# Kernel tuning notes

Measured on AMD Instinct MI355X. Metric: run time of the kernel, lower is better.

## Reference

```python
import jax, jax.numpy as jnp
import numpy as np

B, S, D, H = 4, 2048, 1024, 16
HD = D // H  # head size = 64

def setup_inputs() -> dict:
    key = jax.random.key(0)
    ks = jax.random.split(key, 9)
    s = 1.0 / np.sqrt(D)
    inp = {"x": jax.random.normal(ks[0], (B, S, D), dtype=jnp.float32)}
    for i, n in enumerate(["q", "k", "v", "o"]):
        inp[f"W{n}"] = jax.random.uniform(ks[1 + 2 * i], (D, D), minval=-s, maxval=s, dtype=jnp.float32)
        inp[f"b{n}"] = jax.random.uniform(ks[2 + 2 * i], (D,), minval=-s, maxval=s, dtype=jnp.float32)
    return inp

def reference(x, Wq, bq, Wk, bk, Wv, bv, Wo, bo):
    b, s, d = x.shape
    # project and split heads: [b, h, s, hd]
    def heads(y):
        return y.reshape(b, s, H, HD).transpose(0, 2, 1, 3)
    q = heads(x @ Wq.T + bq)
    k = heads(x @ Wk.T + bk)
    v = heads(x @ Wv.T + bv)
    scores = jnp.einsum('bhqd,bhkd->bhqk', q, k) / jnp.sqrt(jnp.float32(HD))
    attn = jax.nn.softmax(scores, axis=-1)
    ctx = jnp.einsum('bhqk,bhkd->bhqd', attn, v)
    ctx = ctx.transpose(0, 2, 1, 3).reshape(b, s, d)
    return ctx @ Wo.T + bo
```

## Files before the change

### kernel.cpp

```cpp
#include <hip/hip_runtime.h>
#include <hip/hip_bf16.h>

typedef __bf16 bf16;
typedef __bf16 bf16x8 __attribute__((ext_vector_type(8)));
typedef __bf16 bf16x4 __attribute__((ext_vector_type(4)));
typedef float f32x4 __attribute__((ext_vector_type(4)));
typedef float f32x16 __attribute__((ext_vector_type(16)));
typedef unsigned int u32;
typedef u32 u32x4 __attribute__((ext_vector_type(4)));

#define B_ 4
#define S_ 2048
#define D_ 1024
#define H_ 16
#define HD_ 64
#define LOG2E 1.4426950408889634f

static __device__ __forceinline__ f32x4 mfma16(bf16x8 a, bf16x8 b, f32x4 c) {
  return __builtin_amdgcn_mfma_f32_16x16x32_bf16(a, b, c, 0, 0, 0);
}
static __device__ __forceinline__ f32x16 mfma32(bf16x8 a, bf16x8 b, f32x16 c) {
  return __builtin_amdgcn_mfma_f32_32x32x16_bf16(a, b, c, 0, 0, 0);
}
static __device__ __forceinline__ void gload_lds16(const void* g, void* l) {
  __builtin_amdgcn_global_load_lds(
      (const __attribute__((address_space(1))) void*)g,
      (__attribute__((address_space(3))) void*)l, 16, 0, 0);
}
static __device__ __forceinline__ u32 pack2(float lo, float hi) {
  union { bf16 h[2]; u32 u; } un;
  un.h[0] = (bf16)lo; un.h[1] = (bf16)hi;
  return un.u;
}

__global__ void cvt_kernel(const float* __restrict__ in, bf16* __restrict__ out, int n4) {
  int i = blockIdx.x * blockDim.x + threadIdx.x;
  const int stride = gridDim.x * blockDim.x;
  for (; i < n4; i += stride) {
    float4 v = reinterpret_cast<const float4*>(in)[i];
    bf16x4 o;
    o[0] = (bf16)v.x; o[1] = (bf16)v.y; o[2] = (bf16)v.z; o[3] = (bf16)v.w;
    reinterpret_cast<bf16x4*>(out)[i] = o;
  }
}
__global__ void cvtw_kernel(const float* __restrict__ w0, const float* __restrict__ w1,
                            const float* __restrict__ w2, const float* __restrict__ w3,
                            bf16* __restrict__ o0, bf16* __restrict__ o1,
                            bf16* __restrict__ o2, bf16* __restrict__ o3, int n4) {
  const float* in = blockIdx.y == 0 ? w0 : blockIdx.y == 1 ? w1 : blockIdx.y == 2 ? w2 : w3;
  bf16* out = blockIdx.y == 0 ? o0 : blockIdx.y == 1 ? o1 : blockIdx.y == 2 ? o2 : o3;
  const int i = blockIdx.x * blockDim.x + threadIdx.x;
  float4 v = reinterpret_cast<const float4*>(in)[i];
  bf16x4 o;
  o[0] = (bf16)v.x; o[1] = (bf16)v.y; o[2] = (bf16)v.z; o[3] = (bf16)v.w;
  reinterpret_cast<bf16x4*>(out)[i] = o;
}

template<bool OUT_BF16, bool BIAS_ROW>
__global__ __launch_bounds__(512, 2)
void gemm2(const bf16* __restrict__ A, const bf16* __restrict__ W,
           const float* __restrict__ bias, void* __restrict__ Cout,
           int M, int N, int K, float scale) {
  __shared__ __align__(16) char lds[147456];
  const int tid = threadIdx.x;
  const int wave = tid >> 6;
  const int lane = tid & 63;
  const int g = lane >> 4, r16 = lane & 15;
  const int m0 = blockIdx.y * 256, n0 = blockIdx.x * 128;
  const int wm = (wave >> 1) * 64, wn = (wave & 1) * 64;

  f32x4 acc[4][4] = {};

  const int srow = tid >> 3;
  const int scol = ((tid & 7) ^ (srow & 7)) * 8;
  const int wdst = wave * 1024;
  const int nkt = K >> 6;

  auto stage = [&](int bi, int t) {
    char* buf = lds + bi * 49152;
    const int kb = t << 6;
#pragma unroll
    for (int q = 0; q < 4; ++q)
      gload_lds16(&A[(size_t)(m0 + q * 64 + srow) * K + kb + scol],
                  buf + q * 8192 + wdst);
#pragma unroll
    for (int q = 0; q < 2; ++q)
      gload_lds16(&W[(size_t)(n0 + q * 64 + srow) * K + kb + scol],
                  buf + 32768 + q * 8192 + wdst);
  };

  stage(0, 0);
  stage(1, 1);
  int cur = 0;

  for (int t = 0; t < nkt; ++t) {
    if (t + 1 < nkt) asm volatile("s_waitcnt vmcnt(6)" ::: "memory");
    else             asm volatile("s_waitcnt vmcnt(0)" ::: "memory");
    __builtin_amdgcn_s_barrier();
    int nx2 = cur + 2; if (nx2 >= 3) nx2 -= 3;
    if (t + 2 < nkt) stage(nx2, t + 2);

    const char* bufA = lds + cur * 49152;
    const char* bufB = bufA + 32768;
#pragma unroll
    for (int kk = 0; kk < 2; ++kk) {
      bf16x8 af[4], bfr[4];
#pragma unroll
      for (int i = 0; i < 4; ++i) {
        const int ra = wm + i * 16 + r16;
        af[i]  = *reinterpret_cast<const bf16x8*>(
            bufA + ra * 128 + (((4 * kk + g) ^ (ra & 7)) * 16));
        const int rb = wn + i * 16 + r16;
        bfr[i] = *reinterpret_cast<const bf16x8*>(
            bufB + rb * 128 + (((4 * kk + g) ^ (rb & 7)) * 16));
      }
      __builtin_amdgcn_s_setprio(1);
#pragma unroll
      for (int i = 0; i < 4; ++i)
#pragma unroll
        for (int j = 0; j < 4; ++j)
          acc[i][j] = mfma16(af[i], bfr[j], acc[i][j]);
      __builtin_amdgcn_s_setprio(0);
    }
    cur = (cur + 1 == 3) ? 0 : cur + 1;
  }

#pragma unroll
  for (int i = 0; i < 4; ++i) {
#pragma unroll
    for (int j = 0; j < 4; ++j) {
      const int col = n0 + wn + j * 16 + r16;
      float bcol = BIAS_ROW ? 0.f : bias[col];
#pragma unroll
      for (int r = 0; r < 4; ++r) {
        const int row = m0 + wm + i * 16 + g * 4 + r;
        const float bv = BIAS_ROW ? bias[row] : bcol;
        const float v = (acc[i][j][r] + bv) * scale;
        if (OUT_BF16)
          reinterpret_cast<bf16*>(Cout)[(size_t)row * N + col] = (bf16)v;
        else
          reinterpret_cast<float*>(Cout)[(size_t)row * N + col] = v;
      }
    }
  }
}

#define VMB(N) do { asm volatile("s_waitcnt vmcnt(" #N ")" ::: "memory"); \
                    __builtin_amdgcn_s_barrier(); } while (0)

__global__ __launch_bounds__(256, 2)
void attn_kernel(const bf16* __restrict__ Q, const bf16* __restrict__ K,
                 const bf16* __restrict__ Vt, bf16* __restrict__ CTX) {
  const unsigned nwg = gridDim.x * gridDim.y;
  const unsigned lid = blockIdx.x + gridDim.x * blockIdx.y;
  const unsigned swzid = (lid & 7) * (nwg >> 3) + (lid >> 3);
  const int bh = (int)(swzid >> 3);
  const int q0 = (int)(swzid & 7) * 256;
  const int h = bh & (H_ - 1), b = bh >> 4;
  const int tid = threadIdx.x, wave = tid >> 6, lane = tid & 63;
  const int l32 = lane & 31, hi = lane >> 5;

  const bf16* Qb  = Q  + ((size_t)b * S_) * D_ + h * HD_;
  const bf16* Kb  = K  + ((size_t)b * S_) * D_ + h * HD_;
  const bf16* Vtb = Vt + (size_t)(h * HD_) * (B_ * S_) + b * S_;

  __shared__ __align__(16) char lds[65536];
  char* const kb0 = lds;             char* const vb0 = lds + 32768;
  char* const kb1 = lds + 8192;      char* const vb1 = lds + 40960;
  char* const kb2 = lds + 16384;     char* const vb2 = lds + 49152;
  char* const kb3 = lds + 24576;     char* const vb3 = lds + 57344;

  const int qbase = q0 + wave * 64;
  bf16x8 qf0[4], qf1[4];
#pragma unroll
  for (int ks = 0; ks < 4; ++ks) {
    qf0[ks] = *reinterpret_cast<const bf16x8*>(&Qb[(size_t)(qbase + l32) * D_ + ks * 16 + hi * 8]);
    qf1[ks] = *reinterpret_cast<const bf16x8*>(&Qb[(size_t)(qbase + 32 + l32) * D_ + ks * 16 + hi * 8]);
  }

  bf16x8 onesf;
#pragma unroll
  for (int j = 0; j < 8; ++j) onesf[j] = (bf16)1.0f;

  f32x16 ctx00 = {}, ctx01 = {}, ctx10 = {}, ctx11 = {};
  f32x16 lacc0 = {}, lacc1 = {};

  const int krow0 = wave * 16 + (lane >> 3);
  const int xs = ((lane & 7) ^ (lane >> 3)) * 8;
  const int stoff = wave * 2048;
  const int swl = (l32 & 7) << 4;
  int coa[4];
#pragma unroll
  for (int ks = 0; ks < 4; ++ks) coa[ks] = (ks * 32 + hi * 16) ^ swl;
  const int rA = l32 * 128, rB = (32 + l32) * 128;

  const bf16* Kst = Kb  + (size_t)krow0 * D_ + xs;
  const bf16* Vst = Vtb + (size_t)krow0 * (B_ * S_) + xs;

  auto stage = [&](char* kd, char* vd) {
    gload_lds16(Kst,                  kd + stoff);
    gload_lds16(Kst + 8 * D_,         kd + stoff + 1024);
    gload_lds16(Vst,                  vd + stoff);
    gload_lds16(Vst + 8 * (B_ * S_),  vd + stoff + 1024);
    Kst += 64 * D_;
    Vst += 64;
  };

  auto expack = [&](const f32x16& s, u32* w) {
#pragma unroll
    for (int a = 0; a < 4; ++a)
#pragma unroll
      for (int c = 0; c < 2; ++c)
        w[2 * a + c] = pack2(__builtin_amdgcn_exp2f(s[4 * a + 2 * c]),
                             __builtin_amdgcn_exp2f(s[4 * a + 2 * c + 1]));
  };

  auto compute = [&](const char* bK, const char* bV) {
    bf16x8 kf0[4], kf1[4];
#pragma unroll
    for (int ks = 0; ks < 4; ++ks) {
      kf0[ks] = *reinterpret_cast<const bf16x8*>(bK + rA + coa[ks]);
      kf1[ks] = *reinterpret_cast<const bf16x8*>(bK + rB + coa[ks]);
    }
    const f32x16 z = {};
    f32x16 s00, s01;
    __builtin_amdgcn_s_setprio(1);
    s00 = mfma32(kf0[0], qf0[0], z);
    s01 = mfma32(kf1[0], qf0[0], z);
#pragma unroll
    for (int ks = 1; ks < 4; ++ks) {
      s00 = mfma32(kf0[ks], qf0[ks], s00);
      s01 = mfma32(kf1[ks], qf0[ks], s01);
    }
    __builtin_amdgcn_s_setprio(0);
    u32 w00[8], w01[8];
    expack(s00, w00); expack(s01, w01);
    f32x16 s10, s11;
    __builtin_amdgcn_s_setprio(1);
    s10 = mfma32(kf0[0], qf1[0], z);
    s11 = mfma32(kf1[0], qf1[0], z);
#pragma unroll
    for (int ks = 1; ks < 4; ++ks) {
      s10 = mfma32(kf0[ks], qf1[ks], s10);
      s11 = mfma32(kf1[ks], qf1[ks], s11);
    }
    __builtin_amdgcn_s_setprio(0);
    u32 w10[8], w11[8];
    expack(s10, w10); expack(s11, w11);
    bf16x8 vf0[4], vf1[4];
#pragma unroll
    for (int ksp = 0; ksp < 4; ++ksp) {
      vf0[ksp] = *reinterpret_cast<const bf16x8*>(bV + rA + coa[ksp]);
      vf1[ksp] = *reinterpret_cast<const bf16x8*>(bV + rB + coa[ksp]);
    }
#pragma unroll
    for (int m = 0; m < 2; ++m) {
      const u32* wlo = m ? w10 : w00;
      const u32* whi = m ? w11 : w01;
      f32x16& la = m ? lacc1 : lacc0;
      f32x16& c0 = m ? ctx10 : ctx00;
      f32x16& c1 = m ? ctx11 : ctx01;
#pragma unroll
      for (int T = 0; T < 2; ++T) {
        const u32* w = T ? whi : wlo;
#pragma unroll
        for (int k1 = 0; k1 < 2; ++k1) {
          auto rAp = __builtin_amdgcn_permlane32_swap((int)w[4 * k1 + 0], (int)w[4 * k1 + 2], false, false);
          auto rBp = __builtin_amdgcn_permlane32_swap((int)w[4 * k1 + 1], (int)w[4 * k1 + 3], false, false);
          u32x4 fw;
          fw[0] = (u32)rAp[0]; fw[1] = (u32)rBp[0]; fw[2] = (u32)rAp[1]; fw[3] = (u32)rBp[1];
          const bf16x8 pa = __builtin_bit_cast(bf16x8, fw);
          const int ksp = 2 * T + k1;
          __builtin_amdgcn_s_setprio(1);
          la = mfma32(pa, onesf, la);
          c0 = mfma32(pa, vf0[ksp], c0);
          c1 = mfma32(pa, vf1[ksp], c1);
          __builtin_amdgcn_s_setprio(0);
        }
      }
    }
  };

  stage(kb0, vb0);
  stage(kb1, vb1);
  stage(kb2, vb2);

  for (int u = 0; u < 7; ++u) {
    VMB(8); stage(kb3, vb3); compute(kb0, vb0);
    VMB(8); stage(kb0, vb0); compute(kb1, vb1);
    VMB(8); stage(kb1, vb1); compute(kb2, vb2);
    VMB(8); stage(kb2, vb2); compute(kb3, vb3);
  }
  VMB(8); stage(kb3, vb3); compute(kb0, vb0);
  VMB(8); compute(kb1, vb1);
  VMB(4); compute(kb2, vb2);
  VMB(0); compute(kb3, vb3);
  __syncthreads();

  char* Cw = lds + wave * 8192;
#pragma unroll
  for (int rg = 0; rg < 16; ++rg) {
    const int ql = (rg & 3) + 8 * (rg >> 2) + 4 * hi;
    const int swq = (ql & 7) << 4;
    {
      const float inv = 1.0f / lacc0[rg];
      *reinterpret_cast<bf16*>(Cw + ql * 128 + ((l32 * 2) ^ swq)) = (bf16)(ctx00[rg] * inv);
      *reinterpret_cast<bf16*>(Cw + ql * 128 + ((64 + l32 * 2) ^ swq)) = (bf16)(ctx01[rg] * inv);
    }
    {
      const float inv = 1.0f / lacc1[rg];
      *reinterpret_cast<bf16*>(Cw + (32 + ql) * 128 + ((l32 * 2) ^ swq)) = (bf16)(ctx10[rg] * inv);
      *reinterpret_cast<bf16*>(Cw + (32 + ql) * 128 + ((64 + l32 * 2) ^ swq)) = (bf16)(ctx11[rg] * inv);
    }
  }
  asm volatile("" ::: "memory");
#pragma unroll
  for (int i = 0; i < 8; ++i) {
    const int s = i * 64 + lane;
    const int row = s >> 3, cs = (s & 7) * 16;
    bf16x8 v = *reinterpret_cast<const bf16x8*>(Cw + row * 128 + (cs ^ ((row & 7) << 4)));
    *reinterpret_cast<bf16x8*>(
        &CTX[(size_t)(b * S_ + q0 + wave * 64 + row) * D_ + h * HD_ + cs / 2]) = v;
  }
}

extern "C" void kernel_launch(void* const* d_in, const int* in_sizes, int n_in,
                              void* d_out, int out_size, void* d_ws, size_t ws_size,
                              hipStream_t stream) {
  const float* x  = (const float*)d_in[0];
  const float* Wq = (const float*)d_in[1]; const float* bq = (const float*)d_in[2];
  const float* Wk = (const float*)d_in[3]; const float* bk = (const float*)d_in[4];
  const float* Wv = (const float*)d_in[5]; const float* bv = (const float*)d_in[6];
  const float* Wo = (const float*)d_in[7]; const float* bo = (const float*)d_in[8];

  char* ws = (char*)d_ws;
  const size_t MB = 1048576;
  bf16* xb  = (bf16*)(ws);
  bf16* wqb = (bf16*)(ws + 16 * MB);
  bf16* wkb = (bf16*)(ws + 18 * MB);
  bf16* wvb = (bf16*)(ws + 20 * MB);
  bf16* wob = (bf16*)(ws + 22 * MB);
  bf16* qb  = (bf16*)(ws + 24 * MB);
  bf16* kb  = (bf16*)(ws + 40 * MB);
  bf16* vtb = (bf16*)(ws + 56 * MB);
  bf16* ctx = (bf16*)(ws + 72 * MB);

  cvt_kernel<<<2048, 256, 0, stream>>>(x, xb, 2097152);
  cvtw_kernel<<<dim3(1024, 4), 256, 0, stream>>>(Wq, Wk, Wv, Wo, wqb, wkb, wvb, wob, 262144);

  dim3 gq(1024 / 128, 8192 / 256);
  gemm2<true,  false><<<gq, 512, 0, stream>>>(xb, wqb, bq, qb, 8192, 1024, 1024, 0.125f * LOG2E);
  gemm2<true,  false><<<gq, 512, 0, stream>>>(xb, wkb, bk, kb, 8192, 1024, 1024, 1.0f);
  dim3 gv(8192 / 128, 1024 / 256);
  gemm2<true,  true ><<<gv, 512, 0, stream>>>(wvb, xb, bv, vtb, 1024, 8192, 1024, 1.0f);

  attn_kernel<<<dim3(8, 64), 256, 0, stream>>>(qb, kb, vtb, ctx);

  gemm2<false, false><<<gq, 512, 0, stream>>>(ctx, wob, bo, d_out, 8192, 1024, 1024, 1.0f);
}
```

Measured before the change: 193.1 us.

## Retile projection GEMMs to 128x256 with 4 waves and shrink attention pipeline

The projection GEMM moves from a 256x128 tile with 8 waves and K-step 64 to a 128x256 tile with 4 waves, a 64x128 per-wave tile and K-step 32. It halves LDS use, adds an XOR swizzle for 64-byte rows and adds a grouped workgroup-ID swizzle for L2 locality. The attention kernel drops from 4-stage to 3-stage K/V buffering to cut LDS, and its launch bounds rise to 3 blocks per CU for higher occupancy. The risks are register pressure from the larger per-wave accumulator and a shallower prefetch depth in attention.

```diff
diff --git a/kernel.cpp b/kernel.cpp
--- a/kernel.cpp
+++ b/kernel.cpp
@@ -57,36 +57,40 @@
 }
 
 template<bool OUT_BF16, bool BIAS_ROW>
-__global__ __launch_bounds__(512, 2)
-void gemm2(const bf16* __restrict__ A, const bf16* __restrict__ W,
+__global__ __launch_bounds__(256, 2)
+void gemm3(const bf16* __restrict__ A, const bf16* __restrict__ W,
            const float* __restrict__ bias, void* __restrict__ Cout,
            int M, int N, int K, float scale) {
-  __shared__ __align__(16) char lds[147456];
+  __shared__ __align__(16) char lds[73728];
   const int tid = threadIdx.x;
   const int wave = tid >> 6;
   const int lane = tid & 63;
   const int g = lane >> 4, r16 = lane & 15;
-  const int m0 = blockIdx.y * 256, n0 = blockIdx.x * 128;
-  const int wm = (wave >> 1) * 64, wn = (wave & 1) * 64;
-
-  f32x4 acc[4][4] = {};
-
-  const int srow = tid >> 3;
-  const int scol = ((tid & 7) ^ (srow & 7)) * 8;
+  const unsigned nwgx = gridDim.x;
+  const unsigned nwg = nwgx * gridDim.y;
+  unsigned lid = blockIdx.x + nwgx * blockIdx.y;
+  unsigned swz = (lid & 7) * (nwg >> 3) + (lid >> 3);
+  const int m0 = (int)(swz / nwgx) * 128, n0 = (int)(swz % nwgx) * 256;
+  const int wm = (wave >> 1) * 64, wn = (wave & 1) * 128;
+
+  f32x4 acc[4][8] = {};
+
+  const int arow0 = tid >> 2;
+  const int acol = ((tid & 3) ^ ((tid >> 3) & 3)) * 8;
   const int wdst = wave * 1024;
-  const int nkt = K >> 6;
+  const int nkt = K >> 5;
 
   auto stage = [&](int bi, int t) {
-    char* buf = lds + bi * 49152;
-    const int kb = t << 6;
+    char* buf = lds + bi * 24576;
+    const int kb = t << 5;
+#pragma unroll
+    for (int q = 0; q < 2; ++q)
+      gload_lds16(&A[(size_t)(m0 + q * 64 + arow0) * K + kb + acol],
+                  buf + q * 4096 + wdst);
 #pragma unroll
     for (int q = 0; q < 4; ++q)
-      gload_lds16(&A[(size_t)(m0 + q * 64 + srow) * K + kb + scol],
-                  buf + q * 8192 + wdst);
-#pragma unroll
-    for (int q = 0; q < 2; ++q)
-      gload_lds16(&W[(size_t)(n0 + q * 64 + srow) * K + kb + scol],
-                  buf + 32768 + q * 8192 + wdst);
+      gload_lds16(&W[(size_t)(n0 + q * 64 + arow0) * K + kb + acol],
+                  buf + 8192 + q * 4096 + wdst);
   };
 
   stage(0, 0);
@@ -100,35 +104,35 @@
     int nx2 = cur + 2; if (nx2 >= 3) nx2 -= 3;
     if (t + 2 < nkt) stage(nx2, t + 2);
 
-    const char* bufA = lds + cur * 49152;
-    const char* bufB = bufA + 32768;
-#pragma unroll
-    for (int kk = 0; kk < 2; ++kk) {
-      bf16x8 af[4], bfr[4];
-#pragma unroll
-      for (int i = 0; i < 4; ++i) {
-        const int ra = wm + i * 16 + r16;
-        af[i]  = *reinterpret_cast<const bf16x8*>(
-            bufA + ra * 128 + (((4 * kk + g) ^ (ra & 7)) * 16));
-        const int rb = wn + i * 16 + r16;
-        bfr[i] = *reinterpret_cast<const bf16x8*>(
-            bufB + rb * 128 + (((4 * kk + g) ^ (rb & 7)) * 16));
-      }
-      __builtin_amdgcn_s_setprio(1);
-#pragma unroll
-      for (int i = 0; i < 4; ++i)
-#pragma unroll
-        for (int j = 0; j < 4; ++j)
-          acc[i][j] = mfma16(af[i], bfr[j], acc[i][j]);
-      __builtin_amdgcn_s_setprio(0);
-    }
+    const char* bufA = lds + cur * 24576;
+    const char* bufB = bufA + 8192;
+    bf16x8 af[4], bfr[8];
+#pragma unroll
+    for (int i = 0; i < 4; ++i) {
+      const int ra = wm + i * 16 + r16;
+      af[i] = *reinterpret_cast<const bf16x8*>(
+          bufA + ra * 64 + ((g ^ ((ra >> 1) & 3)) << 4));
+    }
+#pragma unroll
+    for (int j = 0; j < 8; ++j) {
+      const int rb = wn + j * 16 + r16;
+      bfr[j] = *reinterpret_cast<const bf16x8*>(
+          bufB + rb * 64 + ((g ^ ((rb >> 1) & 3)) << 4));
+    }
+    __builtin_amdgcn_s_setprio(1);
+#pragma unroll
+    for (int i = 0; i < 4; ++i)
+#pragma unroll
+      for (int j = 0; j < 8; ++j)
+        acc[i][j] = mfma16(af[i], bfr[j], acc[i][j]);
+    __builtin_amdgcn_s_setprio(0);
     cur = (cur + 1 == 3) ? 0 : cur + 1;
   }
 
 #pragma unroll
   for (int i = 0; i < 4; ++i) {
 #pragma unroll
-    for (int j = 0; j < 4; ++j) {
+    for (int j = 0; j < 8; ++j) {
       const int col = n0 + wn + j * 16 + r16;
       float bcol = BIAS_ROW ? 0.f : bias[col];
 #pragma unroll
@@ -148,7 +152,7 @@
 #define VMB(N) do { asm volatile("s_waitcnt vmcnt(" #N ")" ::: "memory"); \
                     __builtin_amdgcn_s_barrier(); } while (0)
 
-__global__ __launch_bounds__(256, 2)
+__global__ __launch_bounds__(256, 3)
 void attn_kernel(const bf16* __restrict__ Q, const bf16* __restrict__ K,
                  const bf16* __restrict__ Vt, bf16* __restrict__ CTX) {
   const unsigned nwg = gridDim.x * gridDim.y;
@@ -164,11 +168,10 @@
   const bf16* Kb  = K  + ((size_t)b * S_) * D_ + h * HD_;
   const bf16* Vtb = Vt + (size_t)(h * HD_) * (B_ * S_) + b * S_;
 
-  __shared__ __align__(16) char lds[65536];
-  char* const kb0 = lds;             char* const vb0 = lds + 32768;
-  char* const kb1 = lds + 8192;      char* const vb1 = lds + 40960;
-  char* const kb2 = lds + 16384;     char* const vb2 = lds + 49152;
-  char* const kb3 = lds + 24576;     char* const vb3 = lds + 57344;
+  __shared__ __align__(16) char lds[49152];
+  char* const kb0 = lds;             char* const vb0 = lds + 24576;
+  char* const kb1 = lds + 8192;      char* const vb1 = lds + 32768;
+  char* const kb2 = lds + 16384;     char* const vb2 = lds + 40960;
 
   const int qbase = q0 + wave * 64;
   bf16x8 qf0[4], qf1[4];
@@ -283,18 +286,14 @@
 
   stage(kb0, vb0);
   stage(kb1, vb1);
-  stage(kb2, vb2);
-
-  for (int u = 0; u < 7; ++u) {
-    VMB(8); stage(kb3, vb3); compute(kb0, vb0);
-    VMB(8); stage(kb0, vb0); compute(kb1, vb1);
-    VMB(8); stage(kb1, vb1); compute(kb2, vb2);
-    VMB(8); stage(kb2, vb2); compute(kb3, vb3);
-  }
-  VMB(8); stage(kb3, vb3); compute(kb0, vb0);
-  VMB(8); compute(kb1, vb1);
-  VMB(4); compute(kb2, vb2);
-  VMB(0); compute(kb3, vb3);
+
+  for (int u = 0; u < 10; ++u) {
+    VMB(4); stage(kb2, vb2); compute(kb0, vb0);
+    VMB(4); stage(kb0, vb0); compute(kb1, vb1);
+    VMB(4); stage(kb1, vb1); compute(kb2, vb2);
+  }
+  VMB(4); compute(kb0, vb0);
+  VMB(0); compute(kb1, vb1);
   __syncthreads();
 
   char* Cw = lds + wave * 8192;
@@ -348,13 +347,13 @@
   cvt_kernel<<<2048, 256, 0, stream>>>(x, xb, 2097152);
   cvtw_kernel<<<dim3(1024, 4), 256, 0, stream>>>(Wq, Wk, Wv, Wo, wqb, wkb, wvb, wob, 262144);
 
-  dim3 gq(1024 / 128, 8192 / 256);
-  gemm2<true,  false><<<gq, 512, 0, stream>>>(xb, wqb, bq, qb, 8192, 1024, 1024, 0.125f * LOG2E);
-  gemm2<true,  false><<<gq, 512, 0, stream>>>(xb, wkb, bk, kb, 8192, 1024, 1024, 1.0f);
-  dim3 gv(8192 / 128, 1024 / 256);
-  gemm2<true,  true ><<<gv, 512, 0, stream>>>(wvb, xb, bv, vtb, 1024, 8192, 1024, 1.0f);
+  dim3 gq(1024 / 256, 8192 / 128);
+  gemm3<true,  false><<<gq, 256, 0, stream>>>(xb, wqb, bq, qb, 8192, 1024, 1024, 0.125f * LOG2E);
+  gemm3<true,  false><<<gq, 256, 0, stream>>>(xb, wkb, bk, kb, 8192, 1024, 1024, 1.0f);
+  dim3 gv(8192 / 256, 1024 / 128);
+  gemm3<true,  true ><<<gv, 256, 0, stream>>>(wvb, xb, bv, vtb, 1024, 8192, 1024, 1.0f);
 
   attn_kernel<<<dim3(8, 64), 256, 0, stream>>>(qb, kb, vtb, ctx);
 
-  gemm2<false, false><<<gq, 512, 0, stream>>>(ctx, wob, bo, d_out, 8192, 1024, 1024, 1.0f);
-}
+  gemm3<false, false><<<gq, 256, 0, stream>>>(ctx, wob, bo, d_out, 8192, 1024, 1024, 1.0f);
+}
```

Result: slower. 368.1 us (+90.7%).
